# Kernel tuning notes

Hardware: AMD Instinct MI355X
Metric: run time of the kernel (lower is better)

## Reference

```python
import jax, jax.numpy as jnp
import numpy as np
from jax import lax


def grouped_linear(x, w):
    # x: [d0, d1, G*ws], w: [G, ws, out_per_group] -> [d0, d1, G*out_per_group]
    d0, d1, _ = x.shape
    G, ws, o = w.shape
    x = x.reshape(d0, d1, G, ws)
    return jnp.einsum('btgi,gio->btgh'.replace('h', 'o'), x, w).reshape(d0, d1, G * o)


def gru_layer(x, w_ih, w_hh, b_ih, b_hh):
    # x: [T, H_in]; w_ih/w_hh: [3, H, H_in]; b_ih/b_hh: [3, H]; gate order (r, z, n)
    ih = jnp.einsum('ti,ghi->tgh', x, w_ih) + b_ih  # input projections for all t at once

    def step(h, ih_t):
        hh = jnp.einsum('i,ghi->gh', h, w_hh) + b_hh
        r = jax.nn.sigmoid(ih_t[0] + hh[0])
        z = jax.nn.sigmoid(ih_t[1] + hh[1])
        n = jnp.tanh(ih_t[2] + r * hh[2])
        h_new = n + z * (h - n)
        return h_new, h_new

    h0 = jnp.zeros((w_hh.shape[1],), x.dtype)
    _, ys = lax.scan(step, h0, ih)
    return ys  # [T, H]


def setup_inputs() -> dict:
    key = jax.random.key(0)
    T, B, H = 8192, 1, 512
    HID, G, L = 512, 8, 2
    C_IN, C_OUT, F, KT = 64, 10, 96, 2
    ks = jax.random.split(key, 17)
    s = jnp.float32(0.05)
    return {
        'emb_tbh': jax.random.normal(ks[0], (T, B, H), jnp.float32),
        'c0': jax.random.normal(ks[1], (B, C_IN, T, F), jnp.float32),
        'lin_in_w': jax.random.normal(ks[2], (G, H // G, HID // G), jnp.float32) * s,
        'gru_w_ih': jax.random.normal(ks[3], (L, 3, HID, HID), jnp.float32) * s,
        'gru_w_hh': jax.random.normal(ks[4], (L, 3, HID, HID), jnp.float32) * s,
        'gru_b_ih': jax.random.normal(ks[5], (L, 3, HID), jnp.float32) * s,
        'gru_b_hh': jax.random.normal(ks[6], (L, 3, HID), jnp.float32) * s,
        'gru_skip_w': jax.random.normal(ks[7], (HID, HID), jnp.float32) * s,
        'gru_skip_b': jax.random.normal(ks[8], (HID,), jnp.float32) * s,
        'lin_out_w': jax.random.normal(ks[9], (G, HID // G, HID // G), jnp.float32) * s,
        'df_skip_w': jax.random.normal(ks[10], (HID, H), jnp.float32) * s,
        'df_skip_b': jax.random.normal(ks[11], (HID,), jnp.float32) * s,
        'fc_a_w': jax.random.normal(ks[12], (1, HID), jnp.float32) * s,
        'fc_a_b': jax.random.normal(ks[13], (1,), jnp.float32) * s,
        'df_out_w': jax.random.normal(ks[14], (G, HID // G, (F * C_OUT) // G), jnp.float32) * s,
        'convp_w': jax.random.normal(ks[15], (C_OUT, C_IN, KT, 1), jnp.float32) * s,
        'convp_b': jax.random.normal(ks[16], (C_OUT,), jnp.float32) * s,
    }


def reference(emb_tbh, c0, lin_in_w, gru_w_ih, gru_w_hh, gru_b_ih, gru_b_hh,
              gru_skip_w, gru_skip_b, lin_out_w, df_skip_w, df_skip_b,
              fc_a_w, fc_a_b, df_out_w, convp_w, convp_b):
    T, B, H = emb_tbh.shape  # B == 1 (manual GRU loop assumes it)
    DF_BINS, DF_OUT_CH = 96, 10

    # --- squeezed GRU: grouped linear_in + ReLU, manual GRU layers, skip, grouped linear_out + ReLU
    x = jax.nn.relu(grouped_linear(emb_tbh, lin_in_w))  # [T, B, HID]
    gru_in = x
    h = x[:, 0, :]  # [T, HID], B == 1
    for l in range(gru_w_ih.shape[0]):
        h = gru_layer(h, gru_w_ih[l], gru_w_hh[l], gru_b_ih[l], gru_b_hh[l])
    x = h[:, None, :]
    x = x + (gru_in @ gru_skip_w.T + gru_skip_b)
    x = jax.nn.relu(grouped_linear(x, lin_out_w))  # [T, B, HID]

    # --- skip from embedding + alpha head
    emb = emb_tbh.reshape(B, T, H)  # B==1: pure relabel of dims
    c = x.reshape(B, T, -1)
    c = c + (emb @ df_skip_w.T + df_skip_b)
    alpha = jax.nn.sigmoid(c @ fc_a_w.T + fc_a_b)  # [B, T, 1]

    # --- df_convp: causal time pad (top=1) + Conv2d kernel (2,1), then permute to [B,T,F,Cout]
    c0p = jnp.pad(c0, ((0, 0), (0, 0), (1, 0), (0, 0)))
    c0c = lax.conv_general_dilated(c0p, convp_w, (1, 1), 'VALID',
                                   dimension_numbers=('NCHW', 'OIHW', 'NCHW'))
    c0c = c0c + convp_b[None, :, None, None]
    c0c = jnp.transpose(c0c, (0, 2, 3, 1))  # [B, T, F, Cout]

    # --- df_out: grouped linear + tanh, reshape to coef grid, add conv pathway
    c = jnp.tanh(grouped_linear(c, df_out_w))  # [B, T, F*Cout]
    c = c.reshape(B, T, DF_BINS, DF_OUT_CH) + c0c
    return (c, alpha)
```

## Files before the change

kernel.cpp:

```cpp
#include <hip/hip_runtime.h>
#include <hip/hip_bf16.h>
#include <cstdint>

#define T_STEPS 8192
#define NWG2 64

__device__ __forceinline__ float sigmoidf_(float v) { return 1.f / (1.f + __expf(-v)); }

__device__ __forceinline__ void acc4(float& acc, const float4& wv, const float4& hv) {
  acc = fmaf(hv.x, wv.x, acc); acc = fmaf(hv.y, wv.y, acc);
  acc = fmaf(hv.z, wv.z, acc); acc = fmaf(hv.w, wv.w, acc);
}

__global__ __launch_bounds__(256) void k_grouped_relu(const float* __restrict__ in,
                                                      const float* __restrict__ W,
                                                      float* __restrict__ out) {
  __shared__ float es[512];
  const int t = blockIdx.x;
  const int tid = threadIdx.x;
  const float* inr = in + (size_t)t * 512;
  ((float2*)es)[tid] = ((const float2*)inr)[tid];
  __syncthreads();
#pragma unroll
  for (int rep = 0; rep < 2; ++rep) {
    int jj = tid + rep * 256;
    int g = jj >> 6, o = jj & 63;
    const float* wp = W + (g << 12) + o;
    const float* ep = es + (g << 6);
    float acc = 0.f;
#pragma unroll 8
    for (int i = 0; i < 64; ++i) acc = fmaf(ep[i], wp[i << 6], acc);
    out[(size_t)t * 512 + jj] = fmaxf(acc, 0.f);
  }
}

__global__ __launch_bounds__(256) void k_gemm_rr(const float* __restrict__ A,
                                                 const float* __restrict__ B,
                                                 const float* __restrict__ bias,
                                                 const float* __restrict__ add,
                                                 float* __restrict__ C, int N) {
  __shared__ float As[64][68];
  __shared__ float Bs[64][68];
  const int bm = blockIdx.x << 6, bn = blockIdx.y << 6;
  const int tid = threadIdx.x;
  const int tx = tid & 15, ty = tid >> 4;
  float acc[4][4] = {};
  for (int k0 = 0; k0 < 512; k0 += 64) {
#pragma unroll
    for (int u = 0; u < 4; ++u) {
      int f4 = (u << 8) + tid;
      int m = f4 >> 4;
      int kq = (f4 & 15) << 2;
      float4 av = *(const float4*)(A + (size_t)(bm + m) * 512 + k0 + kq);
      As[kq + 0][m] = av.x; As[kq + 1][m] = av.y; As[kq + 2][m] = av.z; As[kq + 3][m] = av.w;
      float4 bv = *(const float4*)(B + (size_t)(bn + m) * 512 + k0 + kq);
      Bs[kq + 0][m] = bv.x; Bs[kq + 1][m] = bv.y; Bs[kq + 2][m] = bv.z; Bs[kq + 3][m] = bv.w;
    }
    __syncthreads();
#pragma unroll
    for (int k = 0; k < 64; ++k) {
      float4 a4 = *(const float4*)(&As[k][ty << 2]);
      float4 b4 = *(const float4*)(&Bs[k][tx << 2]);
      float ar[4] = {a4.x, a4.y, a4.z, a4.w};
      float br[4] = {b4.x, b4.y, b4.z, b4.w};
#pragma unroll
      for (int i = 0; i < 4; ++i)
#pragma unroll
        for (int j = 0; j < 4; ++j) acc[i][j] = fmaf(ar[i], br[j], acc[i][j]);
    }
    __syncthreads();
  }
  const int n0 = bn + (tx << 2);
  float4 bsv = *(const float4*)(bias + n0);
#pragma unroll
  for (int i = 0; i < 4; ++i) {
    int m = bm + (ty << 2) + i;
    float4 res;
    res.x = acc[i][0] + bsv.x; res.y = acc[i][1] + bsv.y;
    res.z = acc[i][2] + bsv.z; res.w = acc[i][3] + bsv.w;
    if (add) {
      float4 ad = *(const float4*)(add + (size_t)m * N + n0);
      res.x += ad.x; res.y += ad.y; res.z += ad.z; res.w += ad.w;
    }
    *(float4*)(C + (size_t)m * N + n0) = res;
  }
}

__global__ __launch_bounds__(256, 1) void k_gru_fused(
    const float* __restrict__ ih0,
    const float* __restrict__ Whh0, const float* __restrict__ bhh0,
    const float* __restrict__ Wih1, const float* __restrict__ bih1,
    const float* __restrict__ Whh1, const float* __restrict__ bhh1,
    float* __restrict__ h1seq,
    float* __restrict__ b0,
    float* __restrict__ b1,
    unsigned* __restrict__ flags) {
  const int wg = blockIdx.x, tid = threadIdx.x;
  const int l32 = tid & 31, jl = tid >> 5;
  const int r = (wg << 3) + jl;
  float4 w0r[3][4], w1i[3][4], w1h[3][4];
#pragma unroll
  for (int g = 0; g < 3; ++g)
#pragma unroll
    for (int q = 0; q < 4; ++q) {
      size_t off = ((size_t)g << 18) + ((size_t)r << 9) + (l32 << 2) + (q << 7);
      w0r[g][q] = *(const float4*)(Whh0 + off);
      w1i[g][q] = *(const float4*)(Wih1 + off);
      w1h[g][q] = *(const float4*)(Whh1 + off);
    }
  float bh00 = 0, bh01 = 0, bh02 = 0, bi10 = 0, bi11 = 0, bi12 = 0,
        bh10 = 0, bh11 = 0, bh12 = 0;
  if (l32 == 0) {
    bh00 = bhh0[r]; bh01 = bhh0[512 + r]; bh02 = bhh0[1024 + r];
    bi10 = bih1[r]; bi11 = bih1[512 + r]; bi12 = bih1[1024 + r];
    bh10 = bhh1[r]; bh11 = bhh1[512 + r]; bh12 = bhh1[1024 + r];
  }
  float h0own = 0.f, h1own = 0.f;
  unsigned target = 1;
  for (int t = 0; t <= T_STEPS; ++t) {
    const float* r0 = b0 + (((t + 1) & 1) << 9);
    const float* r1 = b1 + (((t + 1) & 1) << 9);
    float* w0p = b0 + ((t & 1) << 9);
    float* w1p = b1 + ((t & 1) << 9);
    float i0 = 0, i1 = 0, i2 = 0;
    if (l32 == 0 && t < T_STEPS) {
      const float* ihp = ih0 + (size_t)t * 1536 + r;
      i0 = ihp[0]; i1 = ihp[512]; i2 = ihp[1024];
    }
    float4 hv0[4], hv1[4];
#pragma unroll
    for (int q = 0; q < 4; ++q) hv0[q] = *(const float4*)(r0 + (l32 << 2) + (q << 7));
#pragma unroll
    for (int q = 0; q < 4; ++q) hv1[q] = *(const float4*)(r1 + (l32 << 2) + (q << 7));
    float a0 = 0, a1 = 0, a2 = 0;
    float e0 = 0, e1 = 0, e2 = 0;
    float d0 = 0, d1 = 0, d2 = 0;
#pragma unroll
    for (int q = 0; q < 4; ++q) {
      float4 h = hv0[q];
      acc4(a0, w0r[0][q], h); acc4(a1, w0r[1][q], h); acc4(a2, w0r[2][q], h);
      acc4(e0, w1i[0][q], h); acc4(e1, w1i[1][q], h); acc4(e2, w1i[2][q], h);
      float4 g = hv1[q];
      acc4(d0, w1h[0][q], g); acc4(d1, w1h[1][q], g); acc4(d2, w1h[2][q], g);
    }
#pragma unroll
    for (int m = 16; m; m >>= 1) {
      a0 += __shfl_xor(a0, m); a1 += __shfl_xor(a1, m); a2 += __shfl_xor(a2, m);
      e0 += __shfl_xor(e0, m); e1 += __shfl_xor(e1, m); e2 += __shfl_xor(e2, m);
      d0 += __shfl_xor(d0, m); d1 += __shfl_xor(d1, m); d2 += __shfl_xor(d2, m);
    }
    if (l32 == 0) {
      if (t < T_STEPS) {
        float rr = sigmoidf_(i0 + a0 + bh00);
        float zz = sigmoidf_(i1 + a1 + bh01);
        float nn = tanhf(fmaf(rr, a2 + bh02, i2));
        h0own = fmaf(zz, h0own - nn, nn);
        w0p[r] = h0own;
      }
      if (t >= 1) {
        float rr = sigmoidf_(e0 + bi10 + d0 + bh10);
        float zz = sigmoidf_(e1 + bi11 + d1 + bh11);
        float nn = tanhf(fmaf(rr, d2 + bh12, e2 + bi12));
        h1own = fmaf(zz, h1own - nn, nn);
        w1p[r] = h1own;
        h1seq[(size_t)(t - 1) * 512 + r] = h1own;
      }
    }
    if (t == T_STEPS) break;
    __syncthreads();
    if (tid == 0)
      __hip_atomic_store(flags + (wg << 5), target, __ATOMIC_RELEASE,
                         __HIP_MEMORY_SCOPE_AGENT);
    if (tid < NWG2) {
      while (__hip_atomic_load(flags + (tid << 5), __ATOMIC_ACQUIRE,
                               __HIP_MEMORY_SCOPE_AGENT) < target)
        __builtin_amdgcn_s_sleep(1);
    }
    __syncthreads();
    ++target;
  }
}

__global__ __launch_bounds__(256) void k_alpha(const float* __restrict__ c,
                                               const float* __restrict__ w,
                                               const float* __restrict__ b,
                                               float* __restrict__ alpha) {
  const int wave = threadIdx.x >> 6, lane = threadIdx.x & 63;
  const int t = (blockIdx.x << 2) + wave;
  const float* cr = c + (size_t)t * 512;
  float acc = 0.f;
#pragma unroll
  for (int q = 0; q < 8; ++q) acc = fmaf(cr[lane + (q << 6)], w[lane + (q << 6)], acc);
#pragma unroll
  for (int m = 32; m; m >>= 1) acc += __shfl_xor(acc, m);
  if (lane == 0) alpha[t] = sigmoidf_(acc + b[0]);
}

__global__ __launch_bounds__(256) void k_dfout_conv(const float* __restrict__ c,
                                                    const float* __restrict__ Wd,
                                                    const float* __restrict__ c0,
                                                    const float* __restrict__ wc,
                                                    const float* __restrict__ bc,
                                                    float* __restrict__ out) {
  __shared__ float cs[512];
  __shared__ float A0[64 * 96];
  __shared__ float A1[64 * 96];
  __shared__ float wcs[1280];
  __shared__ float cc[960];
  const int t = blockIdx.x, tid = threadIdx.x;
  ((float2*)cs)[tid] = ((const float2*)(c + (size_t)t * 512))[tid];
  for (int idx = tid; idx < 64 * 96; idx += 256) {
    int ci = idx / 96, f = idx - ci * 96;
    size_t base = (size_t)ci * ((size_t)T_STEPS * 96) + (size_t)t * 96 + f;
    A1[idx] = c0[base];
    A0[idx] = (t == 0) ? 0.f : c0[base - 96];
  }
  for (int idx = tid; idx < 1280; idx += 256) wcs[idx] = wc[idx];
  __syncthreads();
  for (int idx = tid; idx < 960; idx += 256) {
    int f = idx / 10, co = idx - f * 10;
    float acc = bc[co];
    const float* w = wcs + (co << 7);
#pragma unroll 16
    for (int ci = 0; ci < 64; ++ci) {
      acc = fmaf(A0[ci * 96 + f], w[ci * 2 + 0], acc);
      acc = fmaf(A1[ci * 96 + f], w[ci * 2 + 1], acc);
    }
    cc[idx] = acc;
  }
  __syncthreads();
  for (int idx = tid; idx < 960; idx += 256) {
    int g = idx / 120, o = idx - g * 120;
    const float* wp = Wd + g * 7680 + o;
    const float* ep = cs + (g << 6);
    float acc = 0.f;
#pragma unroll 16
    for (int i = 0; i < 64; ++i) acc = fmaf(ep[i], wp[i * 120], acc);
    out[(size_t)t * 960 + idx] = tanhf(acc) + cc[idx];
  }
}

extern "C" void kernel_launch(void* const* d_in, const int* in_sizes, int n_in,
                              void* d_out, int out_size, void* d_ws, size_t ws_size,
                              hipStream_t stream) {
  const float* emb       = (const float*)d_in[0];
  const float* c0        = (const float*)d_in[1];
  const float* lin_in_w  = (const float*)d_in[2];
  const float* w_ih      = (const float*)d_in[3];
  const float* w_hh      = (const float*)d_in[4];
  const float* b_ih      = (const float*)d_in[5];
  const float* b_hh      = (const float*)d_in[6];
  const float* skip_w    = (const float*)d_in[7];
  const float* skip_b    = (const float*)d_in[8];
  const float* lin_out_w = (const float*)d_in[9];
  const float* df_skip_w = (const float*)d_in[10];
  const float* df_skip_b = (const float*)d_in[11];
  const float* fc_a_w    = (const float*)d_in[12];
  const float* fc_a_b    = (const float*)d_in[13];
  const float* df_out_w  = (const float*)d_in[14];
  const float* convp_w   = (const float*)d_in[15];
  const float* convp_b   = (const float*)d_in[16];

  const size_t T = T_STEPS;
  float* x    = (float*)d_ws;
  float* ih   = x + T * 512;
  float* h1   = ih + T * 1536;
  float* b0   = h1 + T * 512;
  float* b1   = b0 + 1024;
  unsigned* flags = (unsigned*)(b1 + 1024);
  float* sbuf = ih;
  float* vbuf = ih + T * 512;
  float* cbuf = ih + 2 * T * 512;
  float* outc = (float*)d_out;
  float* outa = outc + T * 960;

  k_grouped_relu<<<T_STEPS, 256, 0, stream>>>(emb, lin_in_w, x);
  k_gemm_rr<<<dim3(128, 24), 256, 0, stream>>>(x, w_ih, b_ih, nullptr, ih, 1536);
  (void)hipMemsetAsync(b0, 0, (1024 + 1024 + NWG2 * 32) * 4, stream);
  k_gru_fused<<<NWG2, 256, 0, stream>>>(ih, w_hh, b_hh,
                                        w_ih + 786432, b_ih + 1536,
                                        w_hh + 786432, b_hh + 1536,
                                        h1, b0, b1, flags);
  k_gemm_rr<<<dim3(128, 8), 256, 0, stream>>>(x, skip_w, skip_b, h1, sbuf, 512);
  k_grouped_relu<<<T_STEPS, 256, 0, stream>>>(sbuf, lin_out_w, vbuf);
  k_gemm_rr<<<dim3(128, 8), 256, 0, stream>>>(emb, df_skip_w, df_skip_b, vbuf, cbuf, 512);
  k_alpha<<<T_STEPS / 4, 256, 0, stream>>>(cbuf, fc_a_w, fc_a_b, outa);
  k_dfout_conv<<<T_STEPS, 256, 0, stream>>>(cbuf, df_out_w, c0, convp_w, convp_b, outc);
  (void)in_sizes; (void)n_in; (void)out_size; (void)ws_size;
}
```

Before: 34.90 ms.

## Replace GRU grid barrier with tagged value-flag ring buffers

Removes the per-step flag barrier (two __syncthreads plus spin on all workgroup flags) in the fused two-layer GRU kernel. Each hidden value is now published as a 64-bit atomic word pairing the float with a step tag, and consumers spin directly on the values they need, with each half-wave polling one layer's buffer and exchanging via shuffles. This cuts the global barrier latency on the sequential critical path, at the cost of wider polled loads, more register pressure and reliance on relaxed atomics for ordering.

```diff
diff --git a/kernel.cpp b/kernel.cpp
--- a/kernel.cpp
+++ b/kernel.cpp
@@ -5,11 +5,12 @@
 #define T_STEPS 8192
 #define NWG2 64
 
+typedef unsigned long long ull;
+
 __device__ __forceinline__ float sigmoidf_(float v) { return 1.f / (1.f + __expf(-v)); }
 
-__device__ __forceinline__ void acc4(float& acc, const float4& wv, const float4& hv) {
-  acc = fmaf(hv.x, wv.x, acc); acc = fmaf(hv.y, wv.y, acc);
-  acc = fmaf(hv.z, wv.z, acc); acc = fmaf(hv.w, wv.w, acc);
+__device__ __forceinline__ ull packpair(float v, unsigned tag) {
+  return ((ull)__float_as_uint(v) << 32) | (ull)tag;
 }
 
 __global__ __launch_bounds__(256) void k_grouped_relu(const float* __restrict__ in,
@@ -92,21 +93,24 @@
     const float* __restrict__ Wih1, const float* __restrict__ bih1,
     const float* __restrict__ Whh1, const float* __restrict__ bhh1,
     float* __restrict__ h1seq,
-    float* __restrict__ b0,
-    float* __restrict__ b1,
-    unsigned* __restrict__ flags) {
+    ull* ring0,
+    ull* ring1) {
   const int wg = blockIdx.x, tid = threadIdx.x;
   const int l32 = tid & 31, jl = tid >> 5;
   const int r = (wg << 3) + jl;
-  float4 w0r[3][4], w1i[3][4], w1h[3][4];
+  const bool isH1 = (tid & 32) != 0;
+  float w0f[3][16], w1if[3][16], w1hf[3][16];
 #pragma unroll
   for (int g = 0; g < 3; ++g)
 #pragma unroll
     for (int q = 0; q < 4; ++q) {
       size_t off = ((size_t)g << 18) + ((size_t)r << 9) + (l32 << 2) + (q << 7);
-      w0r[g][q] = *(const float4*)(Whh0 + off);
-      w1i[g][q] = *(const float4*)(Wih1 + off);
-      w1h[g][q] = *(const float4*)(Whh1 + off);
+      float4 v0 = *(const float4*)(Whh0 + off);
+      float4 v1 = *(const float4*)(Wih1 + off);
+      float4 v2 = *(const float4*)(Whh1 + off);
+      w0f[g][q * 4 + 0] = v0.x; w0f[g][q * 4 + 1] = v0.y; w0f[g][q * 4 + 2] = v0.z; w0f[g][q * 4 + 3] = v0.w;
+      w1if[g][q * 4 + 0] = v1.x; w1if[g][q * 4 + 1] = v1.y; w1if[g][q * 4 + 2] = v1.z; w1if[g][q * 4 + 3] = v1.w;
+      w1hf[g][q * 4 + 0] = v2.x; w1hf[g][q * 4 + 1] = v2.y; w1hf[g][q * 4 + 2] = v2.z; w1hf[g][q * 4 + 3] = v2.w;
     }
   float bh00 = 0, bh01 = 0, bh02 = 0, bi10 = 0, bi11 = 0, bi12 = 0,
         bh10 = 0, bh11 = 0, bh12 = 0;
@@ -116,32 +120,48 @@
     bh10 = bhh1[r]; bh11 = bhh1[512 + r]; bh12 = bhh1[1024 + r];
   }
   float h0own = 0.f, h1own = 0.f;
-  unsigned target = 1;
   for (int t = 0; t <= T_STEPS; ++t) {
-    const float* r0 = b0 + (((t + 1) & 1) << 9);
-    const float* r1 = b1 + (((t + 1) & 1) << 9);
-    float* w0p = b0 + ((t & 1) << 9);
-    float* w1p = b1 + ((t & 1) << 9);
     float i0 = 0, i1 = 0, i2 = 0;
     if (l32 == 0 && t < T_STEPS) {
       const float* ihp = ih0 + (size_t)t * 1536 + r;
       i0 = ihp[0]; i1 = ihp[512]; i2 = ihp[1024];
     }
-    float4 hv0[4], hv1[4];
-#pragma unroll
-    for (int q = 0; q < 4; ++q) hv0[q] = *(const float4*)(r0 + (l32 << 2) + (q << 7));
-#pragma unroll
-    for (int q = 0; q < 4; ++q) hv1[q] = *(const float4*)(r1 + (l32 << 2) + (q << 7));
+    const unsigned exp0 = (unsigned)t;
+    const unsigned exp1 = (t > 0) ? (unsigned)(t - 1) : 0u;
+    ull* sp = isH1 ? (ring1 + ((t & 1) << 9)) : (ring0 + (((t + 1) & 1) << 9));
+    const unsigned expm = isH1 ? exp1 : exp0;
+    ull P[16];
+    while (true) {
+      unsigned bad = 0;
+#pragma unroll
+      for (int q = 0; q < 4; ++q)
+#pragma unroll
+        for (int k = 0; k < 4; ++k) {
+          P[q * 4 + k] = __hip_atomic_load(sp + (l32 << 2) + (q << 7) + k,
+                                           __ATOMIC_RELAXED, __HIP_MEMORY_SCOPE_AGENT);
+        }
+#pragma unroll
+      for (int i = 0; i < 16; ++i) bad |= ((unsigned)P[i]) ^ expm;
+      if (__ballot(bad != 0) == 0ull) break;
+    }
+    __asm__ volatile("" ::: "memory");
+    float hv0v[16], hv1v[16];
+#pragma unroll
+    for (int i = 0; i < 16; ++i) {
+      float mine = __uint_as_float((unsigned)(P[i] >> 32));
+      float other = __shfl_xor(mine, 32);
+      hv0v[i] = isH1 ? other : mine;
+      hv1v[i] = isH1 ? mine : other;
+    }
     float a0 = 0, a1 = 0, a2 = 0;
     float e0 = 0, e1 = 0, e2 = 0;
     float d0 = 0, d1 = 0, d2 = 0;
 #pragma unroll
-    for (int q = 0; q < 4; ++q) {
-      float4 h = hv0[q];
-      acc4(a0, w0r[0][q], h); acc4(a1, w0r[1][q], h); acc4(a2, w0r[2][q], h);
-      acc4(e0, w1i[0][q], h); acc4(e1, w1i[1][q], h); acc4(e2, w1i[2][q], h);
-      float4 g = hv1[q];
-      acc4(d0, w1h[0][q], g); acc4(d1, w1h[1][q], g); acc4(d2, w1h[2][q], g);
+    for (int i = 0; i < 16; ++i) {
+      float h = hv0v[i], g = hv1v[i];
+      a0 = fmaf(h, w0f[0][i], a0); a1 = fmaf(h, w0f[1][i], a1); a2 = fmaf(h, w0f[2][i], a2);
+      e0 = fmaf(h, w1if[0][i], e0); e1 = fmaf(h, w1if[1][i], e1); e2 = fmaf(h, w1if[2][i], e2);
+      d0 = fmaf(g, w1hf[0][i], d0); d1 = fmaf(g, w1hf[1][i], d1); d2 = fmaf(g, w1hf[2][i], d2);
     }
 #pragma unroll
     for (int m = 16; m; m >>= 1) {
@@ -155,29 +175,19 @@
         float zz = sigmoidf_(i1 + a1 + bh01);
         float nn = tanhf(fmaf(rr, a2 + bh02, i2));
         h0own = fmaf(zz, h0own - nn, nn);
-        w0p[r] = h0own;
+        __hip_atomic_store(ring0 + ((t & 1) << 9) + r, packpair(h0own, (unsigned)(t + 1)),
+                           __ATOMIC_RELAXED, __HIP_MEMORY_SCOPE_AGENT);
       }
       if (t >= 1) {
         float rr = sigmoidf_(e0 + bi10 + d0 + bh10);
         float zz = sigmoidf_(e1 + bi11 + d1 + bh11);
         float nn = tanhf(fmaf(rr, d2 + bh12, e2 + bi12));
         h1own = fmaf(zz, h1own - nn, nn);
-        w1p[r] = h1own;
+        __hip_atomic_store(ring1 + (((t + 1) & 1) << 9) + r, packpair(h1own, (unsigned)t),
+                           __ATOMIC_RELAXED, __HIP_MEMORY_SCOPE_AGENT);
         h1seq[(size_t)(t - 1) * 512 + r] = h1own;
       }
     }
-    if (t == T_STEPS) break;
-    __syncthreads();
-    if (tid == 0)
-      __hip_atomic_store(flags + (wg << 5), target, __ATOMIC_RELEASE,
-                         __HIP_MEMORY_SCOPE_AGENT);
-    if (tid < NWG2) {
-      while (__hip_atomic_load(flags + (tid << 5), __ATOMIC_ACQUIRE,
-                               __HIP_MEMORY_SCOPE_AGENT) < target)
-        __builtin_amdgcn_s_sleep(1);
-    }
-    __syncthreads();
-    ++target;
   }
 }
 
@@ -265,9 +275,8 @@
   float* x    = (float*)d_ws;
   float* ih   = x + T * 512;
   float* h1   = ih + T * 1536;
-  float* b0   = h1 + T * 512;
-  float* b1   = b0 + 1024;
-  unsigned* flags = (unsigned*)(b1 + 1024);
+  ull* ring0  = (ull*)(h1 + T * 512);
+  ull* ring1  = ring0 + 1024;
   float* sbuf = ih;
   float* vbuf = ih + T * 512;
   float* cbuf = ih + 2 * T * 512;
@@ -276,11 +285,11 @@
 
   k_grouped_relu<<<T_STEPS, 256, 0, stream>>>(emb, lin_in_w, x);
   k_gemm_rr<<<dim3(128, 24), 256, 0, stream>>>(x, w_ih, b_ih, nullptr, ih, 1536);
-  (void)hipMemsetAsync(b0, 0, (1024 + 1024 + NWG2 * 32) * 4, stream);
+  (void)hipMemsetAsync(ring0, 0, 2048 * sizeof(ull), stream);
   k_gru_fused<<<NWG2, 256, 0, stream>>>(ih, w_hh, b_hh,
                                         w_ih + 786432, b_ih + 1536,
                                         w_hh + 786432, b_hh + 1536,
-                                        h1, b0, b1, flags);
+                                        h1, ring0, ring1);
   k_gemm_rr<<<dim3(128, 8), 256, 0, stream>>>(x, skip_w, skip_b, h1, sbuf, 512);
   k_grouped_relu<<<T_STEPS, 256, 0, stream>>>(sbuf, lin_out_w, vbuf);
   k_gemm_rr<<<dim3(128, 8), 256, 0, stream>>>(emb, df_skip_w, df_skip_b, vbuf, cbuf, 512);
```

Result: slower. 43.29 ms (+24.1%).
